# Optimization experiments

Hardware: AMD Instinct MI355X
Metric: run time of the kernel (lower is better)

Reference implementation:

```python
import jax, jax.numpy as jnp
import numpy as np

N, E, G = 20000, 320000, 64
IN_DIM, HID, HEADS, NCLS = 512, 256, 2, 10
EPS = 1e-5
SLOPE = 0.2


def setup_inputs() -> dict:
    key = jax.random.key(0)
    ks = jax.random.split(key, 24)
    s = 0.02
    inp = {
        "feat": jax.random.normal(ks[0], (N, IN_DIM), jnp.float32),
        "src": jax.random.randint(ks[1], (E,), 0, N, jnp.int32),
        "dst": jax.random.randint(ks[2], (E,), 0, N, jnp.int32),
        "graph_ids": jnp.sort(jax.random.randint(ks[3], (N,), 0, G, jnp.int32)),
        # GATv2Conv params (fc_src, fc_dst, attn)
        "W_src": jax.random.normal(ks[4], (IN_DIM, HEADS * HID), jnp.float32) * s,
        "b_src": jnp.zeros((HEADS * HID,), jnp.float32),
        "W_dst": jax.random.normal(ks[5], (IN_DIM, HEADS * HID), jnp.float32) * s,
        "b_dst": jnp.zeros((HEADS * HID,), jnp.float32),
        "attn": jax.random.normal(ks[6], (HEADS, HID), jnp.float32) * s,
        # skip_lin: input_dim -> 2*hidden
        "W_skip": jax.random.normal(ks[7], (IN_DIM, 2 * HID), jnp.float32) * s,
        "b_skip": jnp.zeros((2 * HID,), jnp.float32),
        # bn1 affine
        "gamma": jnp.ones((2 * HID,), jnp.float32),
        "beta": jnp.zeros((2 * HID,), jnp.float32),
        # dim_reducer
        "W_red": jax.random.normal(ks[8], (2 * HID, HID), jnp.float32) * s,
        "b_red": jnp.zeros((HID,), jnp.float32),
        # attention-pool gate Linear(hidden, 1)
        "w_gate": jax.random.normal(ks[9], (HID, 1), jnp.float32) * s,
        "b_gate": jnp.zeros((1,), jnp.float32),
        # classifier MLP
        "W1": jax.random.normal(ks[10], (HID, HID // 2), jnp.float32) * s,
        "b1": jnp.zeros((HID // 2,), jnp.float32),
        "W2": jax.random.normal(ks[11], (HID // 2, NCLS), jnp.float32) * s,
        "b2": jnp.zeros((NCLS,), jnp.float32),
    }
    return inp


def _gatv2(feat, src, dst, W_src, b_src, W_dst, b_dst, attn):
    # feat_src/feat_dst: [N, H, D]
    fs = (feat @ W_src + b_src).reshape(N, HEADS, HID)
    fd = (feat @ W_dst + b_dst).reshape(N, HEADS, HID)
    fs_e = fs[src]                               # [E, H, D]
    m = jax.nn.leaky_relu(fs_e + fd[dst], SLOPE)  # [E, H, D]
    e = jnp.einsum("ehd,hd->eh", m, attn)         # [E, H]
    # edge softmax grouped by destination node
    e_max = jax.ops.segment_max(e, dst, num_segments=N)          # [N, H]
    e_exp = jnp.exp(e - e_max[dst])                               # [E, H]
    denom = jax.ops.segment_sum(e_exp, dst, num_segments=N)      # [N, H]
    alpha = e_exp / denom[dst]                                    # [E, H]
    out = jax.ops.segment_sum(alpha[:, :, None] * fs_e, dst, num_segments=N)
    return out  # [N, H, D]; zero rows for zero in-degree nodes


def reference(feat, src, dst, graph_ids, W_src, b_src, W_dst, b_dst, attn,
              W_skip, b_skip, gamma, beta, W_red, b_red, w_gate, b_gate,
              W1, b1, W2, b2):
    h1 = jax.nn.elu(_gatv2(feat, src, dst, W_src, b_src, W_dst, b_dst, attn))
    h1 = h1.reshape(N, HEADS * HID)
    h1 = h1 + (feat @ W_skip + b_skip)
    # BatchNorm1d (training-mode batch statistics, biased variance)
    mu = jnp.mean(h1, axis=0)
    var = jnp.mean((h1 - mu) ** 2, axis=0)
    h1 = (h1 - mu) * jax.lax.rsqrt(var + EPS) * gamma + beta
    hr = h1 @ W_red + b_red                      # [N, HID]
    # GlobalAttentionPooling: segment softmax of gate scores over each graph
    gate = hr @ w_gate + b_gate                  # [N, 1]
    g_max = jax.ops.segment_max(gate, graph_ids, num_segments=G)
    g_exp = jnp.exp(gate - g_max[graph_ids])
    g_den = jax.ops.segment_sum(g_exp, graph_ids, num_segments=G)
    a = g_exp / g_den[graph_ids]                 # [N, 1]
    h_g = jax.ops.segment_sum(a * hr, graph_ids, num_segments=G)  # [G, HID]
    # classifier (dropout = identity at inference)
    return jax.nn.relu(h_g @ W1 + b1) @ W2 + b2  # [G, NCLS]
```

## Files before the change

### kernel.cpp

```cpp
#include <hip/hip_runtime.h>
#include <math.h>

#define N_NODES 20000
#define N_EDGES 320000
#define N_GRAPH 64
#define IN_DIM  512
#define HID     256
#define F2      512
#define EPS_BN  1e-5f
#define SLOPE   0.2f
#define SCAN_BLOCKS 79
#define N_RT    157
#define RT_PAD  20096

#define SF_BLOCKS   5024
#define SW_BLOCKS   1024
#define INIT_BLOCKS 79
#define HIST_BLOCKS 1250
#define PREP_BLOCKS (SF_BLOCKS + SW_BLOCKS + INIT_BLOCKS + HIST_BLOCKS)
#define TRIPLE_BLOCKS 1920

typedef unsigned short u16;
typedef __attribute__((ext_vector_type(8))) short bf16x8;
typedef __attribute__((ext_vector_type(4))) float floatx4;
typedef _Float16 f16;
typedef __attribute__((ext_vector_type(2))) f16 f16x2;

__device__ __forceinline__ u16 bf_hi(float x) {
    unsigned int u = __float_as_uint(x);
    return (u16)((u + 0x7fffu + ((u >> 16) & 1u)) >> 16);
}
__device__ __forceinline__ float bf_val(u16 h) {
    return __uint_as_float((unsigned int)h << 16);
}
__device__ __forceinline__ f16x2 h2_from_u32(unsigned int u) {
    return __builtin_bit_cast(f16x2, u);
}
__device__ __forceinline__ unsigned int u32_from_h2(f16x2 h) {
    return __builtin_bit_cast(unsigned int, h);
}

__device__ __forceinline__ void gload16(const u16* g, u16* l) {
    __builtin_amdgcn_global_load_lds(
        (const __attribute__((address_space(1))) void*)g,
        (__attribute__((address_space(3))) void*)l, 16, 0, 0);
}

__global__ __launch_bounds__(256) void prep_kernel(
    const float* __restrict__ feat, u16* __restrict__ Fhi,
    const float* __restrict__ Ws, const float* __restrict__ Wd,
    const float* __restrict__ Wk, const float* __restrict__ Wr,
    u16* __restrict__ Whi, u16* __restrict__ Wlo,
    const int* __restrict__ dst, int* __restrict__ counts,
    int* __restrict__ cursor,
    float* __restrict__ stats, float* __restrict__ h_gnum,
    float* __restrict__ gden, float* __restrict__ gate) {
    __shared__ float t[32][33];
    int b = blockIdx.x;
    int tid = threadIdx.x;
    if (b < SF_BLOCKS) {
        int i = b * 256 + tid;
        size_t base = (size_t)i * 8;
        if (i >= N_NODES * IN_DIM / 8) {
            *(uint4*)(Fhi + base) = make_uint4(0, 0, 0, 0);
            return;
        }
        float4 x0 = *(const float4*)(feat + base);
        float4 x1 = *(const float4*)(feat + base + 4);
        float xs[8] = {x0.x, x0.y, x0.z, x0.w, x1.x, x1.y, x1.z, x1.w};
        union { u16 s[8]; uint4 v; } h;
#pragma unroll
        for (int j = 0; j < 8; j++) h.s[j] = bf_hi(xs[j]);
        *(uint4*)(Fhi + base) = h.v;
    } else if (b < SF_BLOCKS + SW_BLOCKS) {
        int bb = b - SF_BLOCKS;
        int kx = bb & 15, ny = (bb >> 4) & 15, w = bb >> 8;
        int ncols = (w == 3) ? 256 : 512;
        int n0 = ny * 32;
        if (n0 >= ncols) return;
        const float* W = (w == 0) ? Ws : ((w == 1) ? Wd : ((w == 2) ? Wk : Wr));
        size_t obase = (size_t)w * 512 * 512;
        int k0 = kx * 32;
        int tx = tid & 31, ty = tid >> 5;
#pragma unroll
        for (int i = 0; i < 4; i++)
            t[ty * 4 + i][tx] = W[(size_t)(k0 + ty * 4 + i) * ncols + n0 + tx];
        __syncthreads();
#pragma unroll
        for (int i = 0; i < 4; i++) {
            float x = t[tx][ty * 4 + i];
            u16 hh = bf_hi(x);
            size_t o = obase + (size_t)(n0 + ty * 4 + i) * 512 + k0 + tx;
            Whi[o] = hh;
            Wlo[o] = bf_hi(x - bf_val(hh));
        }
    } else if (b < SF_BLOCKS + SW_BLOCKS + INIT_BLOCKS) {
        int i = (b - SF_BLOCKS - SW_BLOCKS) * 256 + tid;
        if (i < N_NODES) { cursor[i] = 0; gate[i] = 0.f; }
        if (i < 1024) stats[i] = 0.f;
        if (i < N_GRAPH * HID) h_gnum[i] = 0.f;
        if (i < N_GRAPH) gden[i] = 0.f;
    } else {
        int e = (b - SF_BLOCKS - SW_BLOCKS - INIT_BLOCKS) * 256 + tid;
        if (e < N_EDGES) atomicAdd(&counts[dst[e]], 1);
    }
}

__global__ __launch_bounds__(256) void gemm_mfma_triple(
    const u16* __restrict__ Fhi, const u16* __restrict__ Wthi,
    const float* __restrict__ b_src, const float* __restrict__ b_dst,
    const float* __restrict__ b_skip,
    u16* __restrict__ FS16, u16* __restrict__ FD16,
    u16* __restrict__ h1hi, u16* __restrict__ h1lo,
    const int* __restrict__ counts, int* __restrict__ row_ptr,
    int* __restrict__ bsum) {
    __shared__ u16 S[2][2][8192];
    int b = blockIdx.x;
    int tid = threadIdx.x;
    if (b >= TRIPLE_BLOCKS) {
        int* buf = (int*)&S[0][0][0];
        int bb = b - TRIPLE_BLOCKS;
        int i = bb * 256 + tid;
        buf[tid] = (i < N_NODES) ? counts[i] : 0;
        __syncthreads();
        for (int off = 1; off < 256; off <<= 1) {
            int t = (tid >= off) ? buf[tid - off] : 0;
            __syncthreads();
            buf[tid] += t;
            __syncthreads();
        }
        if (i < N_NODES) row_ptr[i + 1] = buf[tid];
        if (tid == 255) bsum[bb] = buf[255];
        return;
    }
    int xcd = b & 7, slot = b >> 3;
    int rt = (slot / 12) * 8 + xcd;
    if (rt >= N_RT) return;
    int cw = slot % 12;
    int w_idx = cw >> 2;
    int col0 = (cw & 3) * 128;
    int row0 = rt * 128;
    int lane = tid & 63, wave = tid >> 6;
    int wm = (wave & 1) * 64, wn = (wave >> 1) * 64;
    int quad = lane >> 4, l16 = lane & 15;

    int lrow = lane >> 3;
    int kswz = ((lane & 7) ^ lrow) << 3;
    const u16* aS = Fhi + (size_t)(row0 + wave * 32 + lrow) * 512 + kswz;
    const u16* bS = Wthi + (size_t)w_idx * 512 * 512 +
                    (size_t)(col0 + wave * 32 + lrow) * 512 + kswz;

#define STAGE(buf, kk)                                                        \
    do {                                                                      \
        gload16(aS + (size_t)(kk) * 64,         &S[buf][0][(wave * 4 + 0) * 512]); \
        gload16(bS + (size_t)(kk) * 64,         &S[buf][1][(wave * 4 + 0) * 512]); \
        gload16(aS + 4096 + (size_t)(kk) * 64,  &S[buf][0][(wave * 4 + 1) * 512]); \
        gload16(bS + 4096 + (size_t)(kk) * 64,  &S[buf][1][(wave * 4 + 1) * 512]); \
        gload16(aS + 8192 + (size_t)(kk) * 64,  &S[buf][0][(wave * 4 + 2) * 512]); \
        gload16(bS + 8192 + (size_t)(kk) * 64,  &S[buf][1][(wave * 4 + 2) * 512]); \
        gload16(aS + 12288 + (size_t)(kk) * 64, &S[buf][0][(wave * 4 + 3) * 512]); \
        gload16(bS + 12288 + (size_t)(kk) * 64, &S[buf][1][(wave * 4 + 3) * 512]); \
    } while (0)

    int kx8 = (l16 & 7) << 3;
    int oS0 = (quad * 8) ^ kx8;
    int offA = (wm + l16) * 64;
    int offB = (wn + l16) * 64;

    floatx4 acc[4][4];
#pragma unroll
    for (int i = 0; i < 4; i++)
#pragma unroll
        for (int j = 0; j < 4; j++) acc[i][j] = (floatx4){0.f, 0.f, 0.f, 0.f};

    STAGE(0, 0);
    __syncthreads();

#pragma unroll
    for (int kk = 0; kk < 8; kk++) {
        if (kk < 7) STAGE((kk + 1) & 1, kk + 1);
        const u16* A = &S[kk & 1][0][0];
        const u16* B = &S[kk & 1][1][0];
        bf16x8 bv[4][2];
#pragma unroll
        for (int nt = 0; nt < 4; nt++) {
            bv[nt][0] = *(const bf16x8*)&B[offB + nt * 1024 + oS0];
            bv[nt][1] = *(const bf16x8*)&B[offB + nt * 1024 + (oS0 ^ 32)];
        }
#pragma unroll
        for (int mt = 0; mt < 4; mt++) {
            bf16x8 a0 = *(const bf16x8*)&A[offA + mt * 1024 + oS0];
            bf16x8 a1 = *(const bf16x8*)&A[offA + mt * 1024 + (oS0 ^ 32)];
#pragma unroll
            for (int nt = 0; nt < 4; nt++) {
                acc[mt][nt] = __builtin_amdgcn_mfma_f32_16x16x32_bf16(
                    bv[nt][0], a0, acc[mt][nt], 0, 0, 0);
                acc[mt][nt] = __builtin_amdgcn_mfma_f32_16x16x32_bf16(
                    bv[nt][1], a1, acc[mt][nt], 0, 0, 0);
            }
        }
        __syncthreads();
    }
#undef STAGE

    const float* bias = (w_idx == 0) ? b_src : ((w_idx == 1) ? b_dst : b_skip);
    float4 b4[4];
#pragma unroll
    for (int wt = 0; wt < 4; wt++)
        b4[wt] = *(const float4*)(bias + col0 + wn + wt * 16 + quad * 4);
#pragma unroll
    for (int ft = 0; ft < 4; ft++) {
        int m = row0 + wm + ft * 16 + l16;
        if (m >= N_NODES) continue;
        size_t rb = (size_t)m * 512;
#pragma unroll
        for (int wt = 0; wt < 4; wt++) {
            int nb = col0 + wn + wt * 16 + quad * 4;
            float v0 = acc[ft][wt][0] + b4[wt].x;
            float v1 = acc[ft][wt][1] + b4[wt].y;
            float v2 = acc[ft][wt][2] + b4[wt].z;
            float v3 = acc[ft][wt][3] + b4[wt].w;
            if (w_idx <= 1) {
                f16x2 p0; p0[0] = (f16)v0; p0[1] = (f16)v1;
                f16x2 p1; p1[0] = (f16)v2; p1[1] = (f16)v3;
                uint2 wv;
                wv.x = u32_from_h2(p0);
                wv.y = u32_from_h2(p1);
                if (w_idx == 0) *(uint2*)(FS16 + rb + nb) = wv;
                else            *(uint2*)(FD16 + rb + nb) = wv;
            } else {
                u16 h0 = bf_hi(v0), h1_ = bf_hi(v1), h2 = bf_hi(v2), h3 = bf_hi(v3);
                uint2 wv;
                wv.x = (unsigned)h0 | ((unsigned)h1_ << 16);
                wv.y = (unsigned)h2 | ((unsigned)h3 << 16);
                *(uint2*)(h1hi + rb + nb) = wv;
                uint2 lv;
                lv.x = (unsigned)bf_hi(v0 - bf_val(h0)) | ((unsigned)bf_hi(v1 - bf_val(h1_)) << 16);
                lv.y = (unsigned)bf_hi(v2 - bf_val(h2)) | ((unsigned)bf_hi(v3 - bf_val(h3)) << 16);
                *(uint2*)(h1lo + rb + nb) = lv;
            }
        }
    }
}

__global__ __launch_bounds__(256) void scan_fixup_kernel(
    const int* __restrict__ bsum, int* __restrict__ row_ptr) {
    __shared__ int red[256];
    int b = blockIdx.x, tid = threadIdx.x;
    red[tid] = (tid < b) ? bsum[tid] : 0;
    __syncthreads();
    for (int off = 128; off > 0; off >>= 1) {
        if (tid < off) red[tid] += red[tid + off];
        __syncthreads();
    }
    int offset = red[0];
    int i = b * 256 + tid;
    if (i < N_NODES) row_ptr[i + 1] += offset;
    if (b == 0 && tid == 0) row_ptr[0] = 0;
}

__global__ void scatter_kernel(const int* __restrict__ src, const int* __restrict__ dst,
                               const int* __restrict__ row_ptr,
                               int* __restrict__ cursor, int* __restrict__ csr_src) {
    int e = blockIdx.x * blockDim.x + threadIdx.x;
    if (e < N_EDGES) {
        int d = dst[e];
        int pos = atomicAdd(&cursor[d], 1);
        csr_src[row_ptr[d] + pos] = src[e];
    }
}

__global__ __launch_bounds__(256) void edge_fused_kernel(
    const u16* __restrict__ FS16, const u16* __restrict__ FD16,
    const float* __restrict__ attn, const int* __restrict__ csr_src,
    const int* __restrict__ row_ptr,
    u16* __restrict__ h1hi, u16* __restrict__ h1lo) {
    __shared__ float red[3 * 512];
    __shared__ float den[2];
    int n = blockIdx.x, tid = threadIdx.x;
    int lane = tid & 63, wave = tid >> 6;
    int beg = row_ptr[n], end = row_ptr[n + 1], deg = end - beg;
    if (tid < 2) den[tid] = 0.f;

    f16x2 fd2[4], aw2[4];
    {
        uint4 q = *(const uint4*)(FD16 + (size_t)n * 512 + 8 * lane);
        fd2[0] = h2_from_u32(q.x); fd2[1] = h2_from_u32(q.y);
        fd2[2] = h2_from_u32(q.z); fd2[3] = h2_from_u32(q.w);
        float4 a0 = *(const float4*)(attn + 8 * lane);
        float4 a1 = *(const float4*)(attn + 8 * lane + 4);
        aw2[0][0] = (f16)a0.x; aw2[0][1] = (f16)a0.y;
        aw2[1][0] = (f16)a0.z; aw2[1][1] = (f16)a0.w;
        aw2[2][0] = (f16)a1.x; aw2[2][1] = (f16)a1.y;
        aw2[3][0] = (f16)a1.z; aw2[3][1] = (f16)a1.w;
    }
    __syncthreads();

    const f16x2 sl2 = {(f16)SLOPE, (f16)SLOPE};
    float acc[8] = {0.f, 0.f, 0.f, 0.f, 0.f, 0.f, 0.f, 0.f};
    float dp = 0.f;
    const int* cs = csr_src + beg;
    const u16* FSb = FS16 + 8 * lane;
    for (int j = wave; j < deg; j += 4) {
        int s = cs[j];
        uint4 q = *(const uint4*)(FSb + (size_t)s * 512);
        f16x2 f2[4];
        f2[0] = h2_from_u32(q.x); f2[1] = h2_from_u32(q.y);
        f2[2] = h2_from_u32(q.z); f2[3] = h2_from_u32(q.w);
        float p = 0.f;
#pragma unroll
        for (int k = 0; k < 4; k++) {
            f16x2 sm = f2[k] + fd2[k];
            f16x2 m = __builtin_elementwise_max(sm, sm * sl2);
            p = __builtin_amdgcn_fdot2(m, aw2[k], p, false);
        }
#pragma unroll
        for (int off = 16; off > 0; off >>= 1) p += __shfl_xor(p, off, 64);
        float ex = __expf(p);
#pragma unroll
        for (int k = 0; k < 4; k++) {
            acc[2 * k]     += ex * (float)f2[k][0];
            acc[2 * k + 1] += ex * (float)f2[k][1];
        }
        if ((lane & 31) == 0) dp += ex;
    }
    if ((lane & 31) == 0) atomicAdd(&den[lane >> 5], dp);

    if (wave > 0) {
        float* r = &red[(wave - 1) * 512 + lane * 8];
        *(float4*)(r + 0) = *(float4*)&acc[0];
        *(float4*)(r + 4) = *(float4*)&acc[4];
    }
    __syncthreads();
    if (wave == 0) {
#pragma unroll
        for (int w = 0; w < 3; w++) {
            const float* r = &red[w * 512 + lane * 8];
#pragma unroll
            for (int k = 0; k < 8; k++) acc[k] += r[k];
        }
        float d = (lane < 32) ? den[0] : den[1];
        float inv = d > 0.f ? 1.f / d : 0.f;
        size_t base = (size_t)n * 512 + 8 * lane;
        union { u16 s[8]; uint4 v; } qh, ql;
        qh.v = *(const uint4*)(h1hi + base);
        ql.v = *(const uint4*)(h1lo + base);
#pragma unroll
        for (int k = 0; k < 8; k++) {
            float skip = bf_val(qh.s[k]) + bf_val(ql.s[k]);
            float x = acc[k] * inv;
            x = x > 0.f ? x : expm1f(x);
            float y = x + skip;
            u16 hh = bf_hi(y);
            qh.s[k] = hh;
            ql.s[k] = bf_hi(y - bf_val(hh));
        }
        *(uint4*)(h1hi + base) = qh.v;
        *(uint4*)(h1lo + base) = ql.v;
    }
}

__global__ __launch_bounds__(256) void bn_stats_kernel(const u16* __restrict__ h1hi,
                                                       float* __restrict__ stats,
                                                       int rows_per_block) {
    int tid = threadIdx.x;
    int r0 = blockIdx.x * rows_per_block;
    int r1 = min(r0 + rows_per_block, N_NODES);
    float s0 = 0.f, q0 = 0.f, s1 = 0.f, q1 = 0.f;
    for (int r = r0; r < r1; r++) {
        float a = bf_val(h1hi[(size_t)r * F2 + tid]);
        float b = bf_val(h1hi[(size_t)r * F2 + 256 + tid]);
        s0 += a; q0 += a * a;
        s1 += b; q1 += b * b;
    }
    atomicAdd(&stats[tid], s0);
    atomicAdd(&stats[256 + tid], s1);
    atomicAdd(&stats[512 + tid], q0);
    atomicAdd(&stats[512 + 256 + tid], q1);
}

__global__ __launch_bounds__(256) void bn_fold_kernel(
    const float* __restrict__ stats, const float* __restrict__ gamma,
    const float* __restrict__ beta,
    const u16* __restrict__ Whi3, const u16* __restrict__ Wlo3,
    const float* __restrict__ b_red,
    u16* __restrict__ Wphi, u16* __restrict__ Wplo, float* __restrict__ bias2) {
    __shared__ float sScale[512], sShift[512];
    __shared__ float red[256];
    int n = blockIdx.x, tid = threadIdx.x;
    for (int c = tid; c < 512; c += 256) {
        float mu = stats[c] / (float)N_NODES;
        float var = stats[512 + c] / (float)N_NODES - mu * mu;
        float sc = gamma[c] * rsqrtf(var + EPS_BN);
        sScale[c] = sc;
        sShift[c] = beta[c] - mu * sc;
    }
    __syncthreads();
    float part = 0.f;
    for (int k = tid; k < 512; k += 256) {
        size_t o = (size_t)n * 512 + k;
        float w = bf_val(Whi3[o]) + bf_val(Wlo3[o]);
        part += sShift[k] * w;
        float wp = w * sScale[k];
        u16 hh = bf_hi(wp);
        Wphi[o] = hh;
        Wplo[o] = bf_hi(wp - bf_val(hh));
    }
    red[tid] = part; __syncthreads();
    for (int off = 128; off > 0; off >>= 1) {
        if (tid < off) red[tid] += red[tid + off];
        __syncthreads();
    }
    if (tid == 0) bias2[n] = b_red[n] + red[0];
}

__global__ __launch_bounds__(256) void gemm_mfma_red(
    const u16* __restrict__ Ahi, const u16* __restrict__ Alo,
    const u16* __restrict__ Bhi, const u16* __restrict__ Blo,
    const float* __restrict__ bias2, const float* __restrict__ wg,
    float* __restrict__ hr, float* __restrict__ gate) {
    __shared__ u16 AsHi[128 * 40];
    __shared__ u16 AsLo[128 * 40];
    int tid = threadIdx.x;
    int row0 = blockIdx.x * 128;
    int col0 = blockIdx.y * 128;
    int lane = tid & 63, wave = tid >> 6;
    int wm = (wave & 1) * 64, wn = (wave >> 1) * 64;
    int quad = lane >> 4, l16 = lane & 15;

    int sr = tid >> 1, sh = (tid & 1) * 16;
    int grow = row0 + sr;
    bool ok = grow < N_NODES;
    u16* sH = &AsHi[sr * 40 + sh];
    u16* sL = &AsLo[sr * 40 + sh];

    const u16* bPh[4];
    const u16* bPl[4];
#pragma unroll
    for (int nt = 0; nt < 4; nt++) {
        size_t o = (size_t)(col0 + wn + nt * 16 + l16) * 512 + quad * 8;
        bPh[nt] = Bhi + o;
        bPl[nt] = Blo + o;
    }

    floatx4 acc[4][4];
#pragma unroll
    for (int i = 0; i < 4; i++)
#pragma unroll
        for (int j = 0; j < 4; j++) acc[i][j] = (floatx4){0.f, 0.f, 0.f, 0.f};

    for (int k0 = 0; k0 < 512; k0 += 32) {
        uint4 h0 = make_uint4(0, 0, 0, 0), h1v = h0, l0 = h0, l1 = h0;
        if (ok) {
            const u16* g = Ahi + (size_t)grow * 512 + k0 + sh;
            const u16* gl = Alo + (size_t)grow * 512 + k0 + sh;
            h0 = *(const uint4*)(g);
            h1v = *(const uint4*)(g + 8);
            l0 = *(const uint4*)(gl);
            l1 = *(const uint4*)(gl + 8);
        }
        union { uint4 u; bf16x8 v; } bh[4], bl[4];
#pragma unroll
        for (int nt = 0; nt < 4; nt++) {
            bh[nt].u = *(const uint4*)(bPh[nt] + k0);
            bl[nt].u = *(const uint4*)(bPl[nt] + k0);
        }
        __syncthreads();
        *(uint4*)(sH + 0) = h0;
        *(uint4*)(sH + 8) = h1v;
        *(uint4*)(sL + 0) = l0;
        *(uint4*)(sL + 8) = l1;
        __syncthreads();
#pragma unroll
        for (int mt = 0; mt < 4; mt++) {
            int me = (wm + mt * 16 + l16) * 40 + quad * 8;
            bf16x8 ah = *(const bf16x8*)&AsHi[me];
            bf16x8 al = *(const bf16x8*)&AsLo[me];
#pragma unroll
            for (int nt = 0; nt < 4; nt++) {
                acc[mt][nt] = __builtin_amdgcn_mfma_f32_16x16x32_bf16(bh[nt].v, ah, acc[mt][nt], 0, 0, 0);
                acc[mt][nt] = __builtin_amdgcn_mfma_f32_16x16x32_bf16(bl[nt].v, ah, acc[mt][nt], 0, 0, 0);
                acc[mt][nt] = __builtin_amdgcn_mfma_f32_16x16x32_bf16(bh[nt].v, al, acc[mt][nt], 0, 0, 0);
            }
        }
    }

    float4 b4[4], w4[4];
#pragma unroll
    for (int wt = 0; wt < 4; wt++) {
        int nb = col0 + wn + wt * 16 + quad * 4;
        b4[wt] = *(const float4*)(bias2 + nb);
        w4[wt] = *(const float4*)(wg + nb);
    }
#pragma unroll
    for (int ft = 0; ft < 4; ft++) {
        int m = row0 + wm + ft * 16 + l16;
        bool ok2 = m < N_NODES;
        float g = 0.f;
#pragma unroll
        for (int wt = 0; wt < 4; wt++) {
            float4 v;
            v.x = acc[ft][wt][0] + b4[wt].x;
            v.y = acc[ft][wt][1] + b4[wt].y;
            v.z = acc[ft][wt][2] + b4[wt].z;
            v.w = acc[ft][wt][3] + b4[wt].w;
            g += v.x * w4[wt].x + v.y * w4[wt].y + v.z * w4[wt].z + v.w * w4[wt].w;
            if (ok2) *(float4*)(hr + (size_t)m * HID + col0 + wn + wt * 16 + quad * 4) = v;
        }
        g += __shfl_xor(g, 16, 64);
        g += __shfl_xor(g, 32, 64);
        if (ok2 && lane < 16) atomicAdd(&gate[m], g);
    }
}

__device__ __forceinline__ int lower_bound_dev(const int* a, int n, int v) {
    int lo = 0, hi = n;
    while (lo < hi) {
        int mid = (lo + hi) >> 1;
        if (a[mid] < v) lo = mid + 1; else hi = mid;
    }
    return lo;
}

__global__ __launch_bounds__(256) void pool_partial_kernel(
    const float* __restrict__ hr, const float* __restrict__ gate,
    const int* __restrict__ gids, float* __restrict__ h_gnum,
    float* __restrict__ gden) {
    int b = blockIdx.x;
    int g = b >> 3, part = b & 7;
    int tid = threadIdx.x;
    int start = lower_bound_dev(gids, N_NODES, g);
    int end = lower_bound_dev(gids, N_NODES, g + 1);
    int span = end - start;
    int p_beg = start + (span * part) / 8;
    int p_end = start + (span * (part + 1)) / 8;
    if (p_beg >= p_end) return;
    __shared__ float wa[256];
    __shared__ float red[256];
    float acc = 0.f, denacc = 0.f;
    for (int cbeg = p_beg; cbeg < p_end; cbeg += 256) {
        int c = min(256, p_end - cbeg);
        float e = 0.f;
        if (tid < c) { e = expf(gate[cbeg + tid]); wa[tid] = e; }
        red[tid] = (tid < c) ? e : 0.f;
        __syncthreads();
        for (int off = 128; off > 0; off >>= 1) {
            if (tid < off) red[tid] += red[tid + off];
            __syncthreads();
        }
        denacc += red[0];
        for (int i = 0; i < c; i++) acc += wa[i] * hr[(size_t)(cbeg + i) * HID + tid];
        __syncthreads();
    }
    atomicAdd(&h_gnum[g * HID + tid], acc);
    if (tid == 0) atomicAdd(&gden[g], denacc);
}

__global__ __launch_bounds__(128) void classifier_kernel(
    const float* __restrict__ h_gnum, const float* __restrict__ gden,
    const float* __restrict__ W1, const float* __restrict__ b1,
    const float* __restrict__ W2, const float* __restrict__ b2,
    float* __restrict__ out) {
    int g = blockIdx.x;
    int tid = threadIdx.x;
    __shared__ float hg[256];
    __shared__ float z1[128];
    float d = gden[g];
    float invd = d > 0.f ? 1.f / d : 0.f;
    hg[tid] = h_gnum[g * HID + tid] * invd;
    hg[tid + 128] = h_gnum[g * HID + tid + 128] * invd;
    __syncthreads();
    float a = b1[tid];
#pragma unroll 8
    for (int k = 0; k < 256; k++) a += hg[k] * W1[k * 128 + tid];
    z1[tid] = a > 0.f ? a : 0.f;
    __syncthreads();
    if (tid < 10) {
        float o = b2[tid];
#pragma unroll 8
        for (int j = 0; j < 128; j++) o += z1[j] * W2[j * 10 + tid];
        out[g * 10 + tid] = o;
    }
}

extern "C" void kernel_launch(void* const* d_in, const int* in_sizes, int n_in,
                              void* d_out, int out_size, void* d_ws, size_t ws_size,
                              hipStream_t stream) {
    const float* feat   = (const float*)d_in[0];
    const int*   src    = (const int*)d_in[1];
    const int*   dst    = (const int*)d_in[2];
    const int*   gids   = (const int*)d_in[3];
    const float* W_src  = (const float*)d_in[4];
    const float* b_src  = (const float*)d_in[5];
    const float* W_dst  = (const float*)d_in[6];
    const float* b_dst  = (const float*)d_in[7];
    const float* attn   = (const float*)d_in[8];
    const float* W_skip = (const float*)d_in[9];
    const float* b_skip = (const float*)d_in[10];
    const float* gamma  = (const float*)d_in[11];
    const float* beta   = (const float*)d_in[12];
    const float* W_red  = (const float*)d_in[13];
    const float* b_red  = (const float*)d_in[14];
    const float* w_gate = (const float*)d_in[15];
    const float* W1     = (const float*)d_in[17];
    const float* b1     = (const float*)d_in[18];
    const float* W2     = (const float*)d_in[19];
    const float* b2     = (const float*)d_in[20];
    float* out = (float*)d_out;

    char* p = (char*)d_ws;
    auto alloc = [&](size_t bytes) -> char* {
        char* r = p;
        p += (bytes + 255) & ~(size_t)255;
        return r;
    };
    u16*   FS16     = (u16*)alloc((size_t)N_NODES * F2 * 2);
    u16*   FD16     = (u16*)alloc((size_t)N_NODES * F2 * 2);
    u16*   h1hi     = (u16*)alloc((size_t)N_NODES * F2 * 2);
    u16*   h1lo     = (u16*)alloc((size_t)N_NODES * F2 * 2);
    float* gate     = (float*)alloc((size_t)N_NODES * 4);
    float* stats    = (float*)alloc(1024 * 4);
    float* bias2    = (float*)alloc(256 * 4);
    float* h_gnum   = (float*)alloc((size_t)N_GRAPH * HID * 4);
    float* gden     = (float*)alloc((size_t)N_GRAPH * 4);
    int* counts     = (int*)alloc((size_t)N_NODES * 4);
    int* row_ptr    = (int*)alloc((size_t)(N_NODES + 1) * 4);
    int* cursor     = (int*)alloc((size_t)N_NODES * 4);
    int* csr_src    = (int*)alloc((size_t)N_EDGES * 4);
    int* bsum       = (int*)alloc((size_t)SCAN_BLOCKS * 4);
    u16* Fhi        = (u16*)alloc((size_t)RT_PAD * IN_DIM * 2);
    u16* Wthi       = (u16*)alloc((size_t)4 * 512 * 512 * 2);
    u16* Wtlo       = (u16*)alloc((size_t)4 * 512 * 512 * 2);
    u16* Wphi       = (u16*)alloc((size_t)HID * 512 * 2);
    u16* Wplo       = (u16*)alloc((size_t)HID * 512 * 2);
    float* hr = (float*)Fhi;
    (void)ws_size; (void)in_sizes; (void)n_in; (void)out_size;

    const size_t WSZ = (size_t)512 * 512;

    hipMemsetAsync(counts, 0, (size_t)N_NODES * 4, stream);

    prep_kernel<<<PREP_BLOCKS, 256, 0, stream>>>(
        feat, Fhi, W_src, W_dst, W_skip, W_red, Wthi, Wtlo,
        dst, counts, cursor, stats, h_gnum, gden, gate);

    gemm_mfma_triple<<<TRIPLE_BLOCKS + SCAN_BLOCKS, 256, 0, stream>>>(
        Fhi, Wthi, b_src, b_dst, b_skip, FS16, FD16, h1hi, h1lo,
        counts, row_ptr, bsum);

    scan_fixup_kernel<<<SCAN_BLOCKS, 256, 0, stream>>>(bsum, row_ptr);
    scatter_kernel<<<(N_EDGES + 255) / 256, 256, 0, stream>>>(src, dst, row_ptr, cursor, csr_src);

    edge_fused_kernel<<<N_NODES, 256, 0, stream>>>(
        FS16, FD16, attn, csr_src, row_ptr, h1hi, h1lo);

    bn_stats_kernel<<<500, 256, 0, stream>>>(h1hi, stats, 40);
    bn_fold_kernel<<<HID, 256, 0, stream>>>(
        stats, gamma, beta, Wthi + 3 * WSZ, Wtlo + 3 * WSZ, b_red, Wphi, Wplo, bias2);

    dim3 g256((N_NODES + 127) / 128, 2);
    gemm_mfma_red<<<g256, 256, 0, stream>>>(
        h1hi, h1lo, Wphi, Wplo, bias2, w_gate, hr, gate);

    pool_partial_kernel<<<N_GRAPH * 8, 256, 0, stream>>>(hr, gate, gids, h_gnum, gden);

    classifier_kernel<<<N_GRAPH, 128, 0, stream>>>(h_gnum, gden, W1, b1, W2, b2, out);
}
```

Baseline: 373.1 us.

## Map one wavefront per destination node in GATv2 edge aggregation

```diff
diff --git a/kernel.cpp b/kernel.cpp
--- a/kernel.cpp
+++ b/kernel.cpp
@@ -275,12 +275,10 @@
     const float* __restrict__ attn, const int* __restrict__ csr_src,
     const int* __restrict__ row_ptr,
     u16* __restrict__ h1hi, u16* __restrict__ h1lo) {
-    __shared__ float red[3 * 512];
-    __shared__ float den[2];
-    int n = blockIdx.x, tid = threadIdx.x;
+    int tid = threadIdx.x;
     int lane = tid & 63, wave = tid >> 6;
-    int beg = row_ptr[n], end = row_ptr[n + 1], deg = end - beg;
-    if (tid < 2) den[tid] = 0.f;
+    int n = blockIdx.x * 4 + wave;
+    int beg = row_ptr[n], end = row_ptr[n + 1];
 
     f16x2 fd2[4], aw2[4];
     {
@@ -294,15 +292,49 @@
         aw2[2][0] = (f16)a1.x; aw2[2][1] = (f16)a1.y;
         aw2[3][0] = (f16)a1.z; aw2[3][1] = (f16)a1.w;
     }
-    __syncthreads();
 
     const f16x2 sl2 = {(f16)SLOPE, (f16)SLOPE};
     float acc[8] = {0.f, 0.f, 0.f, 0.f, 0.f, 0.f, 0.f, 0.f};
-    float dp = 0.f;
-    const int* cs = csr_src + beg;
+    float den = 0.f;
     const u16* FSb = FS16 + 8 * lane;
-    for (int j = wave; j < deg; j += 4) {
-        int s = cs[j];
+
+    int j = beg;
+    for (; j + 1 < end; j += 2) {
+        int s0 = csr_src[j];
+        int s1 = csr_src[j + 1];
+        uint4 q0 = *(const uint4*)(FSb + (size_t)s0 * 512);
+        uint4 q1 = *(const uint4*)(FSb + (size_t)s1 * 512);
+        f16x2 f0[4], f1[4];
+        f0[0] = h2_from_u32(q0.x); f0[1] = h2_from_u32(q0.y);
+        f0[2] = h2_from_u32(q0.z); f0[3] = h2_from_u32(q0.w);
+        f1[0] = h2_from_u32(q1.x); f1[1] = h2_from_u32(q1.y);
+        f1[2] = h2_from_u32(q1.z); f1[3] = h2_from_u32(q1.w);
+        float p0 = 0.f, p1 = 0.f;
+#pragma unroll
+        for (int k = 0; k < 4; k++) {
+            f16x2 sm0 = f0[k] + fd2[k];
+            f16x2 m0 = __builtin_elementwise_max(sm0, sm0 * sl2);
+            p0 = __builtin_amdgcn_fdot2(m0, aw2[k], p0, false);
+            f16x2 sm1 = f1[k] + fd2[k];
+            f16x2 m1 = __builtin_elementwise_max(sm1, sm1 * sl2);
+            p1 = __builtin_amdgcn_fdot2(m1, aw2[k], p1, false);
+        }
+#pragma unroll
+        for (int off = 16; off > 0; off >>= 1) {
+            p0 += __shfl_xor(p0, off, 64);
+            p1 += __shfl_xor(p1, off, 64);
+        }
+        float e0 = __expf(p0);
+        float e1 = __expf(p1);
+#pragma unroll
+        for (int k = 0; k < 4; k++) {
+            acc[2 * k]     += e0 * (float)f0[k][0] + e1 * (float)f1[k][0];
+            acc[2 * k + 1] += e0 * (float)f0[k][1] + e1 * (float)f1[k][1];
+        }
+        den += e0 + e1;
+    }
+    if (j < end) {
+        int s = csr_src[j];
         uint4 q = *(const uint4*)(FSb + (size_t)s * 512);
         f16x2 f2[4];
         f2[0] = h2_from_u32(q.x); f2[1] = h2_from_u32(q.y);
@@ -322,42 +354,26 @@
             acc[2 * k]     += ex * (float)f2[k][0];
             acc[2 * k + 1] += ex * (float)f2[k][1];
         }
-        if ((lane & 31) == 0) dp += ex;
-    }
-    if ((lane & 31) == 0) atomicAdd(&den[lane >> 5], dp);
-
-    if (wave > 0) {
-        float* r = &red[(wave - 1) * 512 + lane * 8];
-        *(float4*)(r + 0) = *(float4*)&acc[0];
-        *(float4*)(r + 4) = *(float4*)&acc[4];
-    }
-    __syncthreads();
-    if (wave == 0) {
-#pragma unroll
-        for (int w = 0; w < 3; w++) {
-            const float* r = &red[w * 512 + lane * 8];
-#pragma unroll
-            for (int k = 0; k < 8; k++) acc[k] += r[k];
-        }
-        float d = (lane < 32) ? den[0] : den[1];
-        float inv = d > 0.f ? 1.f / d : 0.f;
-        size_t base = (size_t)n * 512 + 8 * lane;
-        union { u16 s[8]; uint4 v; } qh, ql;
-        qh.v = *(const uint4*)(h1hi + base);
-        ql.v = *(const uint4*)(h1lo + base);
-#pragma unroll
-        for (int k = 0; k < 8; k++) {
-            float skip = bf_val(qh.s[k]) + bf_val(ql.s[k]);
-            float x = acc[k] * inv;
-            x = x > 0.f ? x : expm1f(x);
-            float y = x + skip;
-            u16 hh = bf_hi(y);
-            qh.s[k] = hh;
-            ql.s[k] = bf_hi(y - bf_val(hh));
-        }
-        *(uint4*)(h1hi + base) = qh.v;
-        *(uint4*)(h1lo + base) = ql.v;
-    }
+        den += ex;
+    }
+
+    float inv = den > 0.f ? 1.f / den : 0.f;
+    size_t base = (size_t)n * 512 + 8 * lane;
+    union { u16 s[8]; uint4 v; } qh, ql;
+    qh.v = *(const uint4*)(h1hi + base);
+    ql.v = *(const uint4*)(h1lo + base);
+#pragma unroll
+    for (int k = 0; k < 8; k++) {
+        float skip = bf_val(qh.s[k]) + bf_val(ql.s[k]);
+        float x = acc[k] * inv;
+        x = x > 0.f ? x : expm1f(x);
+        float y = x + skip;
+        u16 hh = bf_hi(y);
+        qh.s[k] = hh;
+        ql.s[k] = bf_hi(y - bf_val(hh));
+    }
+    *(uint4*)(h1hi + base) = qh.v;
+    *(uint4*)(h1lo + base) = ql.v;
 }
 
 __global__ __launch_bounds__(256) void bn_stats_kernel(const u16* __restrict__ h1hi,
@@ -651,7 +667,7 @@
     scan_fixup_kernel<<<SCAN_BLOCKS, 256, 0, stream>>>(bsum, row_ptr);
     scatter_kernel<<<(N_EDGES + 255) / 256, 256, 0, stream>>>(src, dst, row_ptr, cursor, csr_src);
 
-    edge_fused_kernel<<<N_NODES, 256, 0, stream>>>(
+    edge_fused_kernel<<<N_NODES / 4, 256, 0, stream>>>(
         FS16, FD16, attn, csr_src, row_ptr, h1hi, h1lo);
 
     bn_stats_kernel<<<500, 256, 0, stream>>>(h1hi, stats, 40);
```

Result: no change. 373.2 us (+0.0%).
